# Optimization experiments

Hardware: AMD Instinct MI355X
Metric: run time of the kernel (lower is better)

The kernel has to match this reference:

```python
import jax, jax.numpy as jnp
import numpy as np

MAX_WAVELENGTH = 10000.0
NUM_HEADS = 15
NUM_KV_HEADS = 5
HEAD_DIM = 64


def apply_rope(x, positions):
    """RoPE: x [B, L, H, D], positions [B, L] (int)."""
    d_half = x.shape[-1] // 2
    x = x.astype(jnp.float32)
    freq_exponents = (2.0 / x.shape[-1]) * jnp.arange(d_half, dtype=jnp.float32)
    timescale = MAX_WAVELENGTH ** freq_exponents  # [d_half]
    radians = positions[..., None].astype(jnp.float32) / timescale  # [B, L, d_half]
    radians = radians[..., None, :]  # [B, L, 1, d_half]
    sin, cos = jnp.sin(radians), jnp.cos(radians)
    x1, x2 = x[..., :d_half], x[..., d_half:]
    return jnp.concatenate([x1 * cos - x2 * sin, x2 * cos + x1 * sin], axis=-1)


def setup_inputs() -> dict:
    key = jax.random.key(0)
    k1, k2, k3, k4 = jax.random.split(key, 4)
    B, L = 2, 2048
    query_states = jax.random.normal(k1, (B, L, NUM_HEADS, HEAD_DIM), dtype=jnp.float32)
    key_states = jax.random.normal(k2, (B, L, NUM_KV_HEADS, HEAD_DIM), dtype=jnp.float32)
    value_states = jax.random.normal(k3, (B, L, NUM_KV_HEADS, HEAD_DIM), dtype=jnp.float32)
    positions = jnp.sort(jax.random.randint(k4, (B, L), 0, L, dtype=jnp.int32), axis=-1)
    # Causal (prefix-LM) boolean mask [B, L, L]
    attention_mask = jnp.broadcast_to(jnp.tril(jnp.ones((L, L), dtype=bool)), (B, L, L))
    return {
        "query_states": query_states,
        "key_states": key_states,
        "value_states": value_states,
        "positions": positions,
        "attention_mask": attention_mask,
    }


def reference(query_states, key_states, value_states, positions, attention_mask):
    B, L = query_states.shape[0], query_states.shape[1]
    groups = NUM_HEADS // NUM_KV_HEADS  # 3

    # RoPE on Q and K (eager, per original module)
    q = apply_rope(query_states, positions)  # [B, L, 15, 64] fp32
    k = apply_rope(key_states, positions)    # [B, L, 5, 64]  fp32

    # GQA expansion: [B, L, Kv, D] -> [B, L, Kv*groups, D]
    k = jnp.repeat(k, groups, axis=2)
    v = jnp.repeat(value_states, groups, axis=2).astype(jnp.float32)

    # Scores in fp32: [B, H, Lq, Lk]
    scores = jnp.einsum("bqhd,bkhd->bhqk", q, k) * (HEAD_DIM ** -0.5)
    big_neg = jnp.finfo(jnp.float32).min
    scores = jnp.where(attention_mask[:, None, :, :], scores, big_neg)
    probs = jax.nn.softmax(scores, axis=-1)

    out = jnp.einsum("bhqk,bkhd->bqhd", probs, v)  # [B, L, H, D]
    return out.reshape(B, L, NUM_HEADS * HEAD_DIM)  # [B, L, 960]
```

## Files before the change

### kernel.cpp

```cpp
#include <hip/hip_runtime.h>
#include <math.h>

#define NB 2
#define NL 2048
#define NHQ 15
#define NKV 5
#define HD 64
#define NT 32
#define GRP 3
#define PST 72
#define NWB 40
#define CST 68
#define CSLOT (32 * CST + 32)

typedef __attribute__((ext_vector_type(8))) short short8;
typedef __attribute__((ext_vector_type(4))) float floatx4;

#define ROPE_C 0.28782313662425575f
#define QSCALE 0.18033688011116016f


__device__ __forceinline__ ushort f2bf(float x) {
    unsigned u = __builtin_bit_cast(unsigned, x);
    u = (u + 0x7FFFu + ((u >> 16) & 1u)) >> 16;
    return (ushort)u;
}
__device__ __forceinline__ unsigned cvtpk(float a, float b) {
    unsigned r;
    asm("v_cvt_pk_bf16_f32 %0, %1, %2" : "=v"(r) : "v"(a), "v"(b));
    return r;
}

union U8  { short8 v; ushort u[8]; };
union F8  { float4 f4[2]; float f[8]; };

__global__ __launch_bounds__(256)
void prep_kv(const float* __restrict__ K, const float* __restrict__ V,
             const int* __restrict__ pos, ushort* __restrict__ Kr,
             ushort* __restrict__ Vr, float* __restrict__ Tc,
             float* __restrict__ Ts) {
    __shared__ float Vs[64][65];
    const int bid = blockIdx.x, t = threadIdx.x;
    if (bid < NB * NKV * NT) {
        int b = bid / (NKV * NT), rem = bid % (NKV * NT);
        int h = rem / NT, k0 = (rem % NT) * 64;
        int j = t >> 2, c0 = t & 3;
        int row = k0 + j;
        const float* src = K + ((size_t)((b * NL + row) * NKV + h)) * HD;
        int db = c0 * 8;
        F8 x1, x2;
        x1.f4[0] = *(const float4*)&src[db];
        x1.f4[1] = *(const float4*)&src[db + 4];
        x2.f4[0] = *(const float4*)&src[db + 32];
        x2.f4[1] = *(const float4*)&src[db + 36];
        float ps = (float)pos[b * NL + row];
        U8 lo, hi; F8 snv, csv;
#pragma unroll
        for (int i = 0; i < 8; ++i) {
            float inv = __expf((float)(db + i) * -ROPE_C);
            float sn, cs; __sincosf(ps * inv, &sn, &cs);
            snv.f[i] = sn; csv.f[i] = cs;
            lo.u[i] = f2bf(x1.f[i] * cs - x2.f[i] * sn);
            hi.u[i] = f2bf(x2.f[i] * cs + x1.f[i] * sn);
        }
        ushort* dst = Kr + (size_t)bid * 4096;
        *(short8*)&dst[(((j >> 4)) * 64 + c0 * 16 + (j & 15)) * 8]     = lo.v;
        *(short8*)&dst[((4 + (j >> 4)) * 64 + c0 * 16 + (j & 15)) * 8] = hi.v;
        if (rem < NT) {
            float* tcp = Tc + ((size_t)(b * NL + row)) * 32 + db;
            float* tsp = Ts + ((size_t)(b * NL + row)) * 32 + db;
            *(float4*)&tcp[0] = csv.f4[0];
            *(float4*)&tcp[4] = csv.f4[1];
            *(float4*)&tsp[0] = snv.f4[0];
            *(float4*)&tsp[4] = snv.f4[1];
        }
    } else {
        int vb = bid - NB * NKV * NT;
        int b = vb / (NKV * NT), rem = vb % (NKV * NT);
        int h = rem / NT, k0 = (rem % NT) * 64;
#pragma unroll
        for (int it = 0; it < 4; ++it) {
            int e = t + it * 256;
            int j = e >> 4, d4 = (e & 15) * 4;
            *(float4*)&Vs[j][d4] =
                *(const float4*)&V[((size_t)((b * NL + k0 + j) * NKV + h)) * HD + d4];
        }
        __syncthreads();
        ushort* dst = Vr + (size_t)vb * 4096;
#pragma unroll
        for (int it = 0; it < 2; ++it) {
            int o = t + it * 256;
            int d = o >> 3, c = o & 7, j0 = c * 8;
            U8 r;
#pragma unroll
            for (int k = 0; k < 8; ++k) r.u[k] = f2bf(Vs[j0 + k][d]);
            *(short8*)&dst[(((c >> 2) * 4 + (d >> 4)) * 64 + (c & 3) * 16 + (d & 15)) * 8] = r.v;
        }
    }
}

template<bool DIAG>
__device__ __forceinline__ void tile_step(
    int kb, int r0, int l16, int quad, int lane,
    const ushort* Kt0, const ushort* Vt0,
    const short8 (&Qa)[2][2], floatx4 (&O)[2][4], float (&lsum)[2],
    ushort* PbW)
{
    const ushort* kt = Kt0 + (size_t)kb * 4096;
    short8 kc[8];
#pragma unroll
    for (int i = 0; i < 8; ++i)
        kc[i] = *(const short8*)&kt[((size_t)i * 64 + lane) * 8];

    floatx4 S[2][4];
#pragma unroll
    for (int rf = 0; rf < 2; ++rf)
#pragma unroll
        for (int c = 0; c < 4; ++c) S[rf][c] = (floatx4){0.f, 0.f, 0.f, 0.f};
#pragma unroll
    for (int s = 0; s < 2; ++s)
#pragma unroll
        for (int c = 0; c < 4; ++c) {
            short8 kfv = kc[s * 4 + c];
            S[0][c] = __builtin_amdgcn_mfma_f32_16x16x32_bf16(kfv, Qa[0][s], S[0][c], 0, 0, 0);
            S[1][c] = __builtin_amdgcn_mfma_f32_16x16x32_bf16(kfv, Qa[1][s], S[1][c], 0, 0, 0);
        }

#pragma unroll
    for (int rf = 0; rf < 2; ++rf) {
        int qrow = r0 + rf * 16 + l16;
        float acc = 0.f;
#pragma unroll
        for (int c = 0; c < 4; ++c) {
            float pv[4];
#pragma unroll
            for (int r = 0; r < 4; ++r) {
                float sv = S[rf][c][r];
                if (DIAG) {
                    int key = kb * 64 + c * 16 + quad * 4 + r;
                    if (key > qrow) sv = -1e30f;
                }
                pv[r] = exp2f(sv);
                acc += pv[r];
            }
            *(uint2*)&PbW[rf * 16 * PST + l16 * PST + c * 16 + quad * 4] =
                make_uint2(cvtpk(pv[0], pv[1]), cvtpk(pv[2], pv[3]));
        }
        lsum[rf] += acc;
    }

    const ushort* vt = Vt0 + (size_t)kb * 4096;
    short8 vc[8];
#pragma unroll
    for (int i = 0; i < 8; ++i)
        vc[i] = *(const short8*)&vt[((size_t)i * 64 + lane) * 8];

#pragma unroll
    for (int s = 0; s < 2; ++s) {
        short8 pf0 = *(const short8*)&PbW[0 * 16 * PST + l16 * PST + s * 32 + quad * 8];
        short8 pf1 = *(const short8*)&PbW[1 * 16 * PST + l16 * PST + s * 32 + quad * 8];
#pragma unroll
        for (int d = 0; d < 4; ++d) {
            short8 vfv = vc[s * 4 + d];
            O[0][d] = __builtin_amdgcn_mfma_f32_16x16x32_bf16(vfv, pf0, O[0][d], 0, 0, 0);
            O[1][d] = __builtin_amdgcn_mfma_f32_16x16x32_bf16(vfv, pf1, O[1][d], 0, 0, 0);
        }
    }
}

__global__ __launch_bounds__(256, 3)
void attn_flash(const float* __restrict__ Q, const ushort* __restrict__ Kr,
                const ushort* __restrict__ Vr, const float* __restrict__ Tc,
                const float* __restrict__ Ts, float* __restrict__ out) {
    __shared__ __align__(16) unsigned char smem[3 * CSLOT * sizeof(float)];

    const int t = threadIdx.x;
    const int w = t >> 6, lane = t & 63;
    const int l16 = lane & 15, quad = lane >> 4;

    const int bid  = blockIdx.x;
    const int work = (bid & 7) * 150 + (bid >> 3);
    const int bh   = work / NWB;
    const int beta = work % NWB;
    const int b = bh / NHQ, h = bh % NHQ;
    const int kvh = h / GRP;

    int qi, leaderw, nch;
    if (beta < 16)      { qi = 48 + beta; leaderw = 0; nch = 4; }
    else if (beta < 32) {
        if (w < 3)      { qi = 32 + (beta - 16); leaderw = 0; nch = 3; }
        else            { qi = beta - 16;        leaderw = 3; nch = 1; }
    } else {
        int c = beta - 32;
        if (w < 2)      { qi = 16 + 2 * c; leaderw = 0; nch = 2; }
        else            { qi = 17 + 2 * c; leaderw = 2; nch = 2; }
    }
    const int ntw   = (qi >> 1) + 1;
    const int chunk = w - leaderw;
    const int kb0   = (ntw * chunk) / nch;
    const int kb1   = (ntw * (chunk + 1)) / nch;
    const int r0    = qi * 32;

    const ushort* Kt0 = Kr + (size_t)((b * NKV + kvh) * NT) * 4096;
    const ushort* Vt0 = Vr + (size_t)((b * NKV + kvh) * NT) * 4096;
    ushort* PbW = (ushort*)smem + w * 2 * 16 * PST;

    short8 Qa[2][2];
#pragma unroll
    for (int rf = 0; rf < 2; ++rf) {
        int row = r0 + rf * 16 + l16;
        const float* src = Q + ((size_t)((b * NL + row) * NHQ + h)) * HD;
        int db = quad * 8;
        F8 x1, x2, cs8, sn8;
        x1.f4[0] = *(const float4*)&src[db];
        x1.f4[1] = *(const float4*)&src[db + 4];
        x2.f4[0] = *(const float4*)&src[db + 32];
        x2.f4[1] = *(const float4*)&src[db + 36];
        const float* tcp = Tc + ((size_t)(b * NL + row)) * 32 + db;
        const float* tsp = Ts + ((size_t)(b * NL + row)) * 32 + db;
        cs8.f4[0] = *(const float4*)&tcp[0];
        cs8.f4[1] = *(const float4*)&tcp[4];
        sn8.f4[0] = *(const float4*)&tsp[0];
        sn8.f4[1] = *(const float4*)&tsp[4];
        union { short8 v; unsigned u[4]; } lo, hi;
#pragma unroll
        for (int i = 0; i < 8; i += 2) {
            float lo0 = (x1.f[i] * cs8.f[i] - x2.f[i] * sn8.f[i]) * QSCALE;
            float lo1 = (x1.f[i + 1] * cs8.f[i + 1] - x2.f[i + 1] * sn8.f[i + 1]) * QSCALE;
            float hi0 = (x2.f[i] * cs8.f[i] + x1.f[i] * sn8.f[i]) * QSCALE;
            float hi1 = (x2.f[i + 1] * cs8.f[i + 1] + x1.f[i + 1] * sn8.f[i + 1]) * QSCALE;
            lo.u[i >> 1] = cvtpk(lo0, lo1);
            hi.u[i >> 1] = cvtpk(hi0, hi1);
        }
        Qa[rf][0] = lo.v;
        Qa[rf][1] = hi.v;
    }

    floatx4 O[2][4];
    float lsum[2] = {0.f, 0.f};
#pragma unroll
    for (int rf = 0; rf < 2; ++rf)
#pragma unroll
        for (int d = 0; d < 4; ++d) O[rf][d] = (floatx4){0.f, 0.f, 0.f, 0.f};

    const int kbe = (kb1 == ntw) ? ntw - 1 : kb1;
    for (int kb = kb0; kb < kbe; ++kb)
        tile_step<false>(kb, r0, l16, quad, lane, Kt0, Vt0, Qa, O, lsum, PbW);
    if (kb1 == ntw)
        tile_step<true>(ntw - 1, r0, l16, quad, lane, Kt0, Vt0, Qa, O, lsum, PbW);

    float ls[2];
#pragma unroll
    for (int rf = 0; rf < 2; ++rf) {
        float v = lsum[rf];
        v += __shfl_xor(v, 16, 64);
        v += __shfl_xor(v, 32, 64);
        ls[rf] = v;
    }

    __syncthreads();
    float* Cmb = (float*)smem;
    if (chunk > 0) {
        float* slot = Cmb + (size_t)(w - 1) * CSLOT;
#pragma unroll
        for (int rf = 0; rf < 2; ++rf) {
#pragma unroll
            for (int d = 0; d < 4; ++d) {
                *(float4*)&slot[(rf * 16 + l16) * CST + d * 16 + quad * 4] =
                    make_float4(O[rf][d][0], O[rf][d][1], O[rf][d][2], O[rf][d][3]);
            }
            if (quad == 0) slot[32 * CST + rf * 16 + l16] = ls[rf];
        }
    }
    __syncthreads();
    if (chunk == 0) {
        for (int m = 1; m < nch; ++m) {
            const float* slot = Cmb + (size_t)(w + m - 1) * CSLOT;
#pragma unroll
            for (int rf = 0; rf < 2; ++rf) {
#pragma unroll
                for (int d = 0; d < 4; ++d) {
                    float4 x = *(const float4*)&slot[(rf * 16 + l16) * CST + d * 16 + quad * 4];
                    O[rf][d][0] += x.x; O[rf][d][1] += x.y;
                    O[rf][d][2] += x.z; O[rf][d][3] += x.w;
                }
                ls[rf] += slot[32 * CST + rf * 16 + l16];
            }
        }
#pragma unroll
        for (int rf = 0; rf < 2; ++rf) {
            float rinv = 1.0f / ls[rf];
            int qrow = r0 + rf * 16 + l16;
            float* op = out + (size_t)(b * NL + qrow) * (NHQ * HD) + h * HD;
#pragma unroll
            for (int d = 0; d < 4; ++d) {
                float4 o = make_float4(O[rf][d][0] * rinv, O[rf][d][1] * rinv,
                                       O[rf][d][2] * rinv, O[rf][d][3] * rinv);
                *(float4*)&op[d * 16 + quad * 4] = o;
            }
        }
    }
}

extern "C" void kernel_launch(void* const* d_in, const int* in_sizes, int n_in,
                              void* d_out, int out_size, void* d_ws, size_t ws_size,
                              hipStream_t stream) {
    const float* Q   = (const float*)d_in[0];
    const float* K   = (const float*)d_in[1];
    const float* V   = (const float*)d_in[2];
    const int*   pos = (const int*)d_in[3];
    ushort* Kr = (ushort*)d_ws;
    ushort* Vr = Kr + (size_t)NB * NKV * NT * 4096;
    float*  Tc = (float*)(Vr + (size_t)NB * NKV * NT * 4096);
    float*  Ts = Tc + (size_t)NB * NL * 32;
    float*  out = (float*)d_out;

    prep_kv<<<2 * NB * NKV * NT, 256, 0, stream>>>(K, V, pos, Kr, Vr, Tc, Ts);
    attn_flash<<<NB * NHQ * NWB, 256, 0, stream>>>(Q, Kr, Vr, Tc, Ts, out);
}
```

Measured before the change: 134.5 us.

## Process key tiles in pairs to overlap QK MFMAs with softmax and PV

Splits softmax into a helper and adds a paired tile step that loads K for two key blocks up front and issues both QK^T MFMA groups before running softmax and PV for each block in turn. The aim is more independent MFMA and load work in flight per wave, so exp/softmax latency and global load latency are hidden behind matrix ops. Occupancy launch bounds drop from 3 to 2 blocks per CU to leave room for the extra registers, which costs latency hiding across waves. The diagonal-mask handling is moved to the last tile of the last pair or to a single leftover tile.

```diff
diff --git a/kernel.cpp b/kernel.cpp
--- a/kernel.cpp
+++ b/kernel.cpp
@@ -100,32 +100,10 @@
 }
 
 template<bool DIAG>
-__device__ __forceinline__ void tile_step(
-    int kb, int r0, int l16, int quad, int lane,
-    const ushort* Kt0, const ushort* Vt0,
-    const short8 (&Qa)[2][2], floatx4 (&O)[2][4], float (&lsum)[2],
-    ushort* PbW)
+__device__ __forceinline__ void softmax_store(
+    int kb, int r0, int l16, int quad, floatx4 (&S)[2][4],
+    float (&lsum)[2], ushort* PbW)
 {
-    const ushort* kt = Kt0 + (size_t)kb * 4096;
-    short8 kc[8];
-#pragma unroll
-    for (int i = 0; i < 8; ++i)
-        kc[i] = *(const short8*)&kt[((size_t)i * 64 + lane) * 8];
-
-    floatx4 S[2][4];
-#pragma unroll
-    for (int rf = 0; rf < 2; ++rf)
-#pragma unroll
-        for (int c = 0; c < 4; ++c) S[rf][c] = (floatx4){0.f, 0.f, 0.f, 0.f};
-#pragma unroll
-    for (int s = 0; s < 2; ++s)
-#pragma unroll
-        for (int c = 0; c < 4; ++c) {
-            short8 kfv = kc[s * 4 + c];
-            S[0][c] = __builtin_amdgcn_mfma_f32_16x16x32_bf16(kfv, Qa[0][s], S[0][c], 0, 0, 0);
-            S[1][c] = __builtin_amdgcn_mfma_f32_16x16x32_bf16(kfv, Qa[1][s], S[1][c], 0, 0, 0);
-        }
-
 #pragma unroll
     for (int rf = 0; rf < 2; ++rf) {
         int qrow = r0 + rf * 16 + l16;
@@ -148,6 +126,36 @@
         }
         lsum[rf] += acc;
     }
+}
+
+template<bool DIAG>
+__device__ __forceinline__ void tile_step(
+    int kb, int r0, int l16, int quad, int lane,
+    const ushort* Kt0, const ushort* Vt0,
+    const short8 (&Qa)[2][2], floatx4 (&O)[2][4], float (&lsum)[2],
+    ushort* PbW)
+{
+    const ushort* kt = Kt0 + (size_t)kb * 4096;
+    short8 kc[8];
+#pragma unroll
+    for (int i = 0; i < 8; ++i)
+        kc[i] = *(const short8*)&kt[((size_t)i * 64 + lane) * 8];
+
+    floatx4 S[2][4];
+#pragma unroll
+    for (int rf = 0; rf < 2; ++rf)
+#pragma unroll
+        for (int c = 0; c < 4; ++c) S[rf][c] = (floatx4){0.f, 0.f, 0.f, 0.f};
+#pragma unroll
+    for (int s = 0; s < 2; ++s)
+#pragma unroll
+        for (int c = 0; c < 4; ++c) {
+            short8 kfv = kc[s * 4 + c];
+            S[0][c] = __builtin_amdgcn_mfma_f32_16x16x32_bf16(kfv, Qa[0][s], S[0][c], 0, 0, 0);
+            S[1][c] = __builtin_amdgcn_mfma_f32_16x16x32_bf16(kfv, Qa[1][s], S[1][c], 0, 0, 0);
+        }
+
+    softmax_store<DIAG>(kb, r0, l16, quad, S, lsum, PbW);
 
     const ushort* vt = Vt0 + (size_t)kb * 4096;
     short8 vc[8];
@@ -168,7 +176,90 @@
     }
 }
 
-__global__ __launch_bounds__(256, 3)
+template<bool DIAGB>
+__device__ __forceinline__ void tile_pair(
+    int kbA, int kbB, int r0, int l16, int quad, int lane,
+    const ushort* Kt0, const ushort* Vt0,
+    const short8 (&Qa)[2][2], floatx4 (&O)[2][4], float (&lsum)[2],
+    ushort* PbW)
+{
+    const ushort* ktA = Kt0 + (size_t)kbA * 4096;
+    const ushort* ktB = Kt0 + (size_t)kbB * 4096;
+    short8 kcA[8], kcB[8];
+#pragma unroll
+    for (int i = 0; i < 8; ++i)
+        kcA[i] = *(const short8*)&ktA[((size_t)i * 64 + lane) * 8];
+#pragma unroll
+    for (int i = 0; i < 8; ++i)
+        kcB[i] = *(const short8*)&ktB[((size_t)i * 64 + lane) * 8];
+
+    floatx4 SA[2][4], SB[2][4];
+#pragma unroll
+    for (int rf = 0; rf < 2; ++rf)
+#pragma unroll
+        for (int c = 0; c < 4; ++c) {
+            SA[rf][c] = (floatx4){0.f, 0.f, 0.f, 0.f};
+            SB[rf][c] = (floatx4){0.f, 0.f, 0.f, 0.f};
+        }
+#pragma unroll
+    for (int s = 0; s < 2; ++s)
+#pragma unroll
+        for (int c = 0; c < 4; ++c) {
+            short8 ka = kcA[s * 4 + c];
+            SA[0][c] = __builtin_amdgcn_mfma_f32_16x16x32_bf16(ka, Qa[0][s], SA[0][c], 0, 0, 0);
+            SA[1][c] = __builtin_amdgcn_mfma_f32_16x16x32_bf16(ka, Qa[1][s], SA[1][c], 0, 0, 0);
+        }
+#pragma unroll
+    for (int s = 0; s < 2; ++s)
+#pragma unroll
+        for (int c = 0; c < 4; ++c) {
+            short8 kb_ = kcB[s * 4 + c];
+            SB[0][c] = __builtin_amdgcn_mfma_f32_16x16x32_bf16(kb_, Qa[0][s], SB[0][c], 0, 0, 0);
+            SB[1][c] = __builtin_amdgcn_mfma_f32_16x16x32_bf16(kb_, Qa[1][s], SB[1][c], 0, 0, 0);
+        }
+
+    const ushort* vtA = Vt0 + (size_t)kbA * 4096;
+    short8 vcA[8];
+#pragma unroll
+    for (int i = 0; i < 8; ++i)
+        vcA[i] = *(const short8*)&vtA[((size_t)i * 64 + lane) * 8];
+
+    softmax_store<false>(kbA, r0, l16, quad, SA, lsum, PbW);
+
+#pragma unroll
+    for (int s = 0; s < 2; ++s) {
+        short8 pf0 = *(const short8*)&PbW[0 * 16 * PST + l16 * PST + s * 32 + quad * 8];
+        short8 pf1 = *(const short8*)&PbW[1 * 16 * PST + l16 * PST + s * 32 + quad * 8];
+#pragma unroll
+        for (int d = 0; d < 4; ++d) {
+            short8 vfv = vcA[s * 4 + d];
+            O[0][d] = __builtin_amdgcn_mfma_f32_16x16x32_bf16(vfv, pf0, O[0][d], 0, 0, 0);
+            O[1][d] = __builtin_amdgcn_mfma_f32_16x16x32_bf16(vfv, pf1, O[1][d], 0, 0, 0);
+        }
+    }
+
+    const ushort* vtB = Vt0 + (size_t)kbB * 4096;
+    short8 vcB[8];
+#pragma unroll
+    for (int i = 0; i < 8; ++i)
+        vcB[i] = *(const short8*)&vtB[((size_t)i * 64 + lane) * 8];
+
+    softmax_store<DIAGB>(kbB, r0, l16, quad, SB, lsum, PbW);
+
+#pragma unroll
+    for (int s = 0; s < 2; ++s) {
+        short8 pf0 = *(const short8*)&PbW[0 * 16 * PST + l16 * PST + s * 32 + quad * 8];
+        short8 pf1 = *(const short8*)&PbW[1 * 16 * PST + l16 * PST + s * 32 + quad * 8];
+#pragma unroll
+        for (int d = 0; d < 4; ++d) {
+            short8 vfv = vcB[s * 4 + d];
+            O[0][d] = __builtin_amdgcn_mfma_f32_16x16x32_bf16(vfv, pf0, O[0][d], 0, 0, 0);
+            O[1][d] = __builtin_amdgcn_mfma_f32_16x16x32_bf16(vfv, pf1, O[1][d], 0, 0, 0);
+        }
+    }
+}
+
+__global__ __launch_bounds__(256, 2)
 void attn_flash(const float* __restrict__ Q, const ushort* __restrict__ Kr,
                 const ushort* __restrict__ Vr, const float* __restrict__ Tc,
                 const float* __restrict__ Ts, float* __restrict__ out) {
@@ -243,11 +334,21 @@
 #pragma unroll
         for (int d = 0; d < 4; ++d) O[rf][d] = (floatx4){0.f, 0.f, 0.f, 0.f};
 
-    const int kbe = (kb1 == ntw) ? ntw - 1 : kb1;
-    for (int kb = kb0; kb < kbe; ++kb)
-        tile_step<false>(kb, r0, l16, quad, lane, Kt0, Vt0, Qa, O, lsum, PbW);
-    if (kb1 == ntw)
-        tile_step<true>(ntw - 1, r0, l16, quad, lane, Kt0, Vt0, Qa, O, lsum, PbW);
+    const bool hasDiag = (kb1 == ntw);
+    int kb = kb0, rem = kb1 - kb0;
+    while (rem >= 2) {
+        if (hasDiag && rem == 2)
+            tile_pair<true>(kb, kb + 1, r0, l16, quad, lane, Kt0, Vt0, Qa, O, lsum, PbW);
+        else
+            tile_pair<false>(kb, kb + 1, r0, l16, quad, lane, Kt0, Vt0, Qa, O, lsum, PbW);
+        kb += 2; rem -= 2;
+    }
+    if (rem == 1) {
+        if (hasDiag)
+            tile_step<true>(kb, r0, l16, quad, lane, Kt0, Vt0, Qa, O, lsum, PbW);
+        else
+            tile_step<false>(kb, r0, l16, quad, lane, Kt0, Vt0, Qa, O, lsum, PbW);
+    }
 
     float ls[2];
 #pragma unroll
```

New measurement: 140.1 us. 4.1% more time.
